# Kernel tuning notes

Hardware: AMD Instinct MI355X
Metric: run time of the kernel (lower is better)

Reference implementation:

```python
import jax, jax.numpy as jnp
import numpy as np
from math import sqrt

HEADS = 16
D_MODEL = 1024
HEAD_DIM = D_MODEL // HEADS  # 64
B, SEQ = 2, 2048


def setup_inputs() -> dict:
    key = jax.random.key(0)
    ks = jax.random.split(key, 8)
    k = jax.random.normal(ks[0], (B, SEQ, D_MODEL), dtype=jnp.float32)
    q = jax.random.normal(ks[1], (B, SEQ, D_MODEL), dtype=jnp.float32)
    v = jax.random.normal(ks[2], (B, SEQ, D_MODEL), dtype=jnp.float32)
    # causal mask, broadcast over batch and heads; masked_fill where mask == 0
    mask = jnp.tril(jnp.ones((SEQ, SEQ), dtype=jnp.int32))[None, None, :, :]
    s = 1.0 / sqrt(HEAD_DIM)
    Wq = jax.random.normal(ks[3], (HEAD_DIM, HEAD_DIM), dtype=jnp.float32) * s
    Wk = jax.random.normal(ks[4], (HEAD_DIM, HEAD_DIM), dtype=jnp.float32) * s
    Wv = jax.random.normal(ks[5], (HEAD_DIM, HEAD_DIM), dtype=jnp.float32) * s
    Wo = jax.random.normal(ks[6], (D_MODEL, D_MODEL), dtype=jnp.float32) * (1.0 / sqrt(D_MODEL))
    bo = jax.random.normal(ks[7], (D_MODEL,), dtype=jnp.float32) * 0.01
    return {"key": k, "query": q, "value": v, "mask": mask,
            "Wq": Wq, "Wk": Wk, "Wv": Wv, "Wo": Wo, "bo": bo}


def reference(key, query, value, mask, Wq, Wk, Wv, Wo, bo):
    b, q_len, d = query.shape
    k_len = key.shape[1]
    hd = d // HEADS
    # reshape to [b, len, heads, head_dim]
    k = key.reshape(b, k_len, HEADS, hd)
    q = query.reshape(b, q_len, HEADS, hd)
    v = value.reshape(b, k_len, HEADS, hd)
    # per-head-dim Linear (weights shared across heads); torch Linear: y = x @ W.T
    k = jnp.einsum('bkhd,ed->bkhe', k, Wk)
    q = jnp.einsum('bqhd,ed->bqhe', q, Wq)
    v = jnp.einsum('bvhd,ed->bvhe', v, Wv)
    # full attention matrix [b, h, q, k]
    product = jnp.einsum('bqhd,bkhd->bhqk', q, k)
    # NOTE: original masks BEFORE scaling by 1/sqrt(head_dim)
    product = jnp.where(mask == 0, jnp.float32(-1e20), product)
    product = product / jnp.float32(sqrt(hd))
    score = jax.nn.softmax(product, axis=-1)
    out = jnp.einsum('bhqv,bvhd->bqhd', score, v).reshape(b, q_len, d)
    out = out @ Wo.T + bo
    return out
```

## Files before the change

kernel.cpp:

```cpp
#include <hip/hip_runtime.h>

typedef __bf16 bf16x8 __attribute__((ext_vector_type(8)));
typedef float  f32x4  __attribute__((ext_vector_type(4)));
typedef unsigned int uint32x4 __attribute__((ext_vector_type(4)));

#define MFMA16(a, b, c) __builtin_amdgcn_mfma_f32_16x16x32_bf16((a), (b), (c), 0, 0, 0)

constexpr int SEQ = 2048;
constexpr int DM  = 1024;
constexpr int NH  = 16;
constexpr int HD  = 64;
constexpr int BATCH = 2;


__device__ inline bf16x8 ld8_f32(const float* p) {
    f32x4 a = *(const f32x4*)p;
    f32x4 b = *(const f32x4*)(p + 4);
    bf16x8 r;
    r[0] = (__bf16)a[0]; r[1] = (__bf16)a[1]; r[2] = (__bf16)a[2]; r[3] = (__bf16)a[3];
    r[4] = (__bf16)b[0]; r[5] = (__bf16)b[1]; r[6] = (__bf16)b[2]; r[7] = (__bf16)b[3];
    return r;
}

__global__ __launch_bounds__(256)
void proj_kernel(const float* __restrict__ Xq, const float* __restrict__ Xk,
                 const float* __restrict__ Xv,
                 const float* __restrict__ Wq, const float* __restrict__ Wk,
                 const float* __restrict__ Wv,
                 __bf16* __restrict__ Qp, __bf16* __restrict__ Kp,
                 __bf16* __restrict__ Vp)
{
    const int tid  = threadIdx.x;
    const int w    = tid >> 6;
    const int lane = tid & 63;
    const int quad = lane >> 4;
    const int l16  = lane & 15;
    const int sblk = blockIdx.x;
    const int bh   = blockIdx.y;
    const int tz   = blockIdx.z;

    const float* X = (tz == 0) ? Xq : (tz == 1) ? Xk : Xv;
    const float* W = (tz == 0) ? Wq : (tz == 1) ? Wk : Wv;
    __bf16*      O = (tz == 0) ? Qp : (tz == 1) ? Kp : Vp;
    const float scale = (tz == 0) ? (0.125f * 1.44269504088896f) : 1.0f;

    const int b = bh >> 4, h = bh & 15;
    const int mrow = sblk * 64 + w * 16 + l16;

    const size_t xoff = (size_t)(b * SEQ + mrow) * DM + h * HD + quad * 8;
    bf16x8 a0 = ld8_f32(X + xoff);
    bf16x8 a1 = ld8_f32(X + xoff + 32);

    f32x4 acc[4];
    #pragma unroll
    for (int nt = 0; nt < 4; ++nt) {
        const size_t woff = (size_t)(nt * 16 + l16) * HD + quad * 8;
        bf16x8 b0 = ld8_f32(W + woff);
        bf16x8 b1 = ld8_f32(W + woff + 32);
        f32x4 c = {0.f, 0.f, 0.f, 0.f};
        c = MFMA16(a0, b0, c);
        c = MFMA16(a1, b1, c);
        acc[nt] = c;
    }

    __bf16* obase = O + (size_t)bh * SEQ * HD;
    #pragma unroll
    for (int nt = 0; nt < 4; ++nt) {
        #pragma unroll
        for (int r = 0; r < 4; ++r) {
            const int srow = sblk * 64 + w * 16 + quad * 4 + r;
            obase[(size_t)srow * HD + nt * 16 + l16] = (__bf16)(acc[nt][r] * scale);
        }
    }
}

__global__ __launch_bounds__(256, 2)
void attn_kernel(const __bf16* __restrict__ Qp, const __bf16* __restrict__ Kp,
                 const __bf16* __restrict__ Vp, __bf16* __restrict__ AO)
{
    __shared__ __align__(16) unsigned int K_lds[2][64 * 36];
    __shared__ __align__(16) unsigned int VT2[2][64 * 36];
    __shared__ __align__(16) __bf16 P_lds[4][16 * 72];

    const int tid  = threadIdx.x;
    const int w    = tid >> 6;
    const int lane = tid & 63;
    const int quad = lane >> 4;
    const int l16  = lane & 15;
    const int pr   = blockIdx.x;
    const int bh   = blockIdx.y;

    const __bf16* Qb = Qp + (size_t)bh * SEQ * HD;
    const __bf16* Kb = Kp + (size_t)bh * SEQ * HD;
    const __bf16* Vb = Vp + (size_t)bh * SEQ * HD;

    bf16x8 onesf;
    #pragma unroll
    for (int i = 0; i < 8; ++i) onesf[i] = (l16 == 0) ? (__bf16)1.0f : (__bf16)0.0f;

    const int krow = tid >> 3, kcol = tid & 7;
    const int jp = tid & 31, d0 = (tid >> 5) * 8;

    #pragma unroll
    for (int phase = 0; phase < 2; ++phase) {
        const int tile = (phase == 0) ? (31 - pr) : pr;
        const int q0   = tile * 64;
        const int nkc  = tile + 1;

        __syncthreads();

        const int mrow = q0 + w * 16 + l16;
        bf16x8 qa0 = *(const bf16x8*)(Qb + (size_t)mrow * HD + quad * 8);
        bf16x8 qa1 = *(const bf16x8*)(Qb + (size_t)mrow * HD + quad * 8 + 32);

        f32x4 accO[4];
        #pragma unroll
        for (int nt = 0; nt < 4; ++nt) { f32x4 z = {0.f,0.f,0.f,0.f}; accO[nt] = z; }
        f32x4 acc5 = {0.f, 0.f, 0.f, 0.f};

        uint32x4 kpre0 = *(const uint32x4*)(Kb + (size_t)krow * HD + kcol * 8);
        uint32x4 kpre1 = *(const uint32x4*)(Kb + (size_t)(krow + 32) * HD + kcol * 8);
        uint32x4 vlo   = *(const uint32x4*)(Vb + (size_t)(2 * jp) * HD + d0);
        uint32x4 vhi   = *(const uint32x4*)(Vb + (size_t)(2 * jp + 1) * HD + d0);

        for (int kc = 0; kc < nkc; ++kc) {
            const int buf = kc & 1;
            *(uint32x4*)&K_lds[buf][krow * 36 + kcol * 4]        = kpre0;
            *(uint32x4*)&K_lds[buf][(krow + 32) * 36 + kcol * 4] = kpre1;
            #pragma unroll
            for (int i2 = 0; i2 < 4; ++i2) {
                const unsigned int va = vlo[i2], vb = vhi[i2];
                VT2[buf][(d0 + 2 * i2    ) * 36 + jp] = (va & 0xffffu) | (vb << 16);
                VT2[buf][(d0 + 2 * i2 + 1) * 36 + jp] = (va >> 16) | (vb & 0xffff0000u);
            }
            __syncthreads();

            if (kc + 1 < nkc) {
                const size_t o = (size_t)(kc + 1) * 64;
                kpre0 = *(const uint32x4*)(Kb + (o + krow) * HD + kcol * 8);
                kpre1 = *(const uint32x4*)(Kb + (o + krow + 32) * HD + kcol * 8);
                vlo   = *(const uint32x4*)(Vb + (o + 2 * jp) * HD + d0);
                vhi   = *(const uint32x4*)(Vb + (o + 2 * jp + 1) * HD + d0);
            }

            f32x4 s[4];
            #pragma unroll
            for (int nt = 0; nt < 4; ++nt) {
                const unsigned int* kb = &K_lds[buf][(nt * 16 + l16) * 36 + quad * 4];
                bf16x8 kb0 = *(const bf16x8*)(kb);
                bf16x8 kb1 = *(const bf16x8*)(kb + 16);
                f32x4 c = {0.f, 0.f, 0.f, 0.f};
                c = MFMA16(qa0, kb0, c);
                c = MFMA16(qa1, kb1, c);
                s[nt] = c;
            }
            if (kc == tile) {
                #pragma unroll
                for (int nt = 0; nt < 4; ++nt) {
                    const int j = kc * 64 + nt * 16 + l16;
                    #pragma unroll
                    for (int r = 0; r < 4; ++r) {
                        const int qrow = q0 + w * 16 + quad * 4 + r;
                        if (j > qrow) s[nt][r] = -1e30f;
                    }
                }
            }
            #pragma unroll
            for (int nt = 0; nt < 4; ++nt) {
                #pragma unroll
                for (int r = 0; r < 4; ++r) {
                    P_lds[w][(quad * 4 + r) * 72 + nt * 16 + l16] =
                        (__bf16)exp2f(s[nt][r]);
                }
            }
            asm volatile("" ::: "memory");
            bf16x8 pa0 = *(const bf16x8*)&P_lds[w][l16 * 72 + quad * 8];
            bf16x8 pa1 = *(const bf16x8*)&P_lds[w][l16 * 72 + quad * 8 + 32];
            #pragma unroll
            for (int nt = 0; nt < 4; ++nt) {
                const unsigned int* vb2 = &VT2[buf][(nt * 16 + l16) * 36 + quad * 4];
                bf16x8 vb0 = *(const bf16x8*)(vb2);
                bf16x8 vb1 = *(const bf16x8*)(vb2 + 16);
                accO[nt] = MFMA16(pa0, vb0, accO[nt]);
                accO[nt] = MFMA16(pa1, vb1, accO[nt]);
            }
            acc5 = MFMA16(pa0, onesf, acc5);
            acc5 = MFMA16(pa1, onesf, acc5);
        }

        const int b = bh >> 4, h = bh & 15;
        float inv[4];
        #pragma unroll
        for (int r = 0; r < 4; ++r) {
            const float ls = __shfl(acc5[r], quad * 16, 64);
            inv[r] = 1.0f / ls;
        }
        #pragma unroll
        for (int nt = 0; nt < 4; ++nt) {
            #pragma unroll
            for (int r = 0; r < 4; ++r) {
                const int qrow = q0 + w * 16 + quad * 4 + r;
                AO[(size_t)(b * SEQ + qrow) * DM + h * HD + nt * 16 + l16] =
                    (__bf16)(accO[nt][r] * inv[r]);
            }
        }
    }
}

__global__ __launch_bounds__(256)
void wconv_kernel(const float* __restrict__ Wo, __bf16* __restrict__ Wb)
{
    const size_t i = ((size_t)blockIdx.x * 256 + threadIdx.x) * 8;
    *(bf16x8*)(Wb + i) = ld8_f32(Wo + i);
}

__global__ __launch_bounds__(256)
void ogemm_kernel(const __bf16* __restrict__ AO, const __bf16* __restrict__ Wb,
                  const float* __restrict__ bo, float* __restrict__ out)
{
    __shared__ __align__(16) unsigned int A_lds[2][64 * 36];
    __shared__ __align__(16) unsigned int B_lds[2][128 * 36];

    const int tid  = threadIdx.x;
    const int w    = tid >> 6;
    const int lane = tid & 63;
    const int quad = lane >> 4;
    const int l16  = lane & 15;
    const int m0   = blockIdx.x * 64;
    const int n0   = blockIdx.y * 128;

    const int row = tid >> 3, c = tid & 7;

    f32x4 acc[8];
    #pragma unroll
    for (int nt = 0; nt < 8; ++nt) { f32x4 z = {0.f,0.f,0.f,0.f}; acc[nt] = z; }

    uint32x4 apre[2], bpre[4];
    #pragma unroll
    for (int i = 0; i < 2; ++i)
        apre[i] = *(const uint32x4*)(AO + (size_t)(m0 + row + i * 32) * DM + c * 8);
    #pragma unroll
    for (int i = 0; i < 4; ++i)
        bpre[i] = *(const uint32x4*)(Wb + (size_t)(n0 + row + i * 32) * DM + c * 8);

    for (int kc = 0; kc < DM / 64; ++kc) {
        const int buf = kc & 1;
        #pragma unroll
        for (int i = 0; i < 2; ++i)
            *(uint32x4*)&A_lds[buf][(row + i * 32) * 36 + c * 4] = apre[i];
        #pragma unroll
        for (int i = 0; i < 4; ++i)
            *(uint32x4*)&B_lds[buf][(row + i * 32) * 36 + c * 4] = bpre[i];
        __syncthreads();

        if (kc + 1 < DM / 64) {
            const size_t o = (size_t)(kc + 1) * 64;
            #pragma unroll
            for (int i = 0; i < 2; ++i)
                apre[i] = *(const uint32x4*)(AO + (size_t)(m0 + row + i * 32) * DM + o + c * 8);
            #pragma unroll
            for (int i = 0; i < 4; ++i)
                bpre[i] = *(const uint32x4*)(Wb + (size_t)(n0 + row + i * 32) * DM + o + c * 8);
        }

        #pragma unroll
        for (int ks = 0; ks < 2; ++ks) {
            bf16x8 a = *(const bf16x8*)&A_lds[buf][(w * 16 + l16) * 36 + ks * 16 + quad * 4];
            #pragma unroll
            for (int nt = 0; nt < 8; ++nt) {
                bf16x8 bb = *(const bf16x8*)&B_lds[buf][(nt * 16 + l16) * 36 + ks * 16 + quad * 4];
                acc[nt] = MFMA16(a, bb, acc[nt]);
            }
        }
    }

    #pragma unroll
    for (int nt = 0; nt < 8; ++nt) {
        const int n = n0 + nt * 16 + l16;
        const float bof = bo[n];
        #pragma unroll
        for (int r = 0; r < 4; ++r) {
            const int m = m0 + w * 16 + quad * 4 + r;
            out[(size_t)m * DM + n] = acc[nt][r] + bof;
        }
    }
}

extern "C" void kernel_launch(void* const* d_in, const int* in_sizes, int n_in,
                              void* d_out, int out_size, void* d_ws, size_t ws_size,
                              hipStream_t stream)
{
    const float* key   = (const float*)d_in[0];
    const float* query = (const float*)d_in[1];
    const float* value = (const float*)d_in[2];
    const float* Wq = (const float*)d_in[4];
    const float* Wk = (const float*)d_in[5];
    const float* Wv = (const float*)d_in[6];
    const float* Wo = (const float*)d_in[7];
    const float* bo = (const float*)d_in[8];

    const size_t per = (size_t)BATCH * NH * SEQ * HD;
    __bf16* Qp = (__bf16*)d_ws;
    __bf16* Kp = Qp + per;
    __bf16* Vp = Kp + per;
    __bf16* AO = Vp + per;
    __bf16* Wb = Kp;

    proj_kernel<<<dim3(SEQ / 64, BATCH * NH, 3), 256, 0, stream>>>(
        query, key, value, Wq, Wk, Wv, Qp, Kp, Vp);
    attn_kernel<<<dim3(SEQ / 128, BATCH * NH), 256, 0, stream>>>(Qp, Kp, Vp, AO);
    wconv_kernel<<<dim3(DM * DM / (256 * 8)), 256, 0, stream>>>(Wo, Wb);
    ogemm_kernel<<<dim3(BATCH * SEQ / 64, DM / 128), 256, 0, stream>>>(
        AO, Wb, bo, (float*)d_out);
}
```

Baseline: 196.5 us.

## Switch attention to 32x32 MFMA with register-resident P and split-K warps

After: 194.6 us. Within noise of the previous version (-1.0%).

```diff
diff --git a/kernel.cpp b/kernel.cpp
--- a/kernel.cpp
+++ b/kernel.cpp
@@ -2,16 +2,20 @@
 
 typedef __bf16 bf16x8 __attribute__((ext_vector_type(8)));
 typedef float  f32x4  __attribute__((ext_vector_type(4)));
+typedef float  f32x16 __attribute__((ext_vector_type(16)));
 typedef unsigned int uint32x4 __attribute__((ext_vector_type(4)));
 
 #define MFMA16(a, b, c) __builtin_amdgcn_mfma_f32_16x16x32_bf16((a), (b), (c), 0, 0, 0)
+#define MFMA32(a, b, c) __builtin_amdgcn_mfma_f32_32x32x16_bf16((a), (b), (c), 0, 0, 0)
+
+#define CVTPK(d, x, y) asm("v_cvt_pk_bf16_f32 %0, %1, %2" : "=v"(d) : "v"(x), "v"(y))
+#define PLSWAP(a, b)   asm("v_permlane32_swap_b32 %0, %1" : "+v"(a), "+v"(b))
 
 constexpr int SEQ = 2048;
 constexpr int DM  = 1024;
 constexpr int NH  = 16;
 constexpr int HD  = 64;
 constexpr int BATCH = 2;
-
 
 __device__ inline bf16x8 ld8_f32(const float* p) {
     f32x4 a = *(const f32x4*)p;
@@ -80,23 +84,20 @@
 {
     __shared__ __align__(16) unsigned int K_lds[2][64 * 36];
     __shared__ __align__(16) unsigned int VT2[2][64 * 36];
-    __shared__ __align__(16) __bf16 P_lds[4][16 * 72];
 
     const int tid  = threadIdx.x;
     const int w    = tid >> 6;
     const int lane = tid & 63;
-    const int quad = lane >> 4;
-    const int l16  = lane & 15;
+    const int hi   = lane >> 5;
+    const int l32  = lane & 31;
+    const int qg   = w >> 1;
+    const int kg   = w & 1;
     const int pr   = blockIdx.x;
     const int bh   = blockIdx.y;
 
     const __bf16* Qb = Qp + (size_t)bh * SEQ * HD;
     const __bf16* Kb = Kp + (size_t)bh * SEQ * HD;
     const __bf16* Vb = Vp + (size_t)bh * SEQ * HD;
-
-    bf16x8 onesf;
-    #pragma unroll
-    for (int i = 0; i < 8; ++i) onesf[i] = (l16 == 0) ? (__bf16)1.0f : (__bf16)0.0f;
 
     const int krow = tid >> 3, kcol = tid & 7;
     const int jp = tid & 31, d0 = (tid >> 5) * 8;
@@ -109,14 +110,19 @@
 
         __syncthreads();
 
-        const int mrow = q0 + w * 16 + l16;
-        bf16x8 qa0 = *(const bf16x8*)(Qb + (size_t)mrow * HD + quad * 8);
-        bf16x8 qa1 = *(const bf16x8*)(Qb + (size_t)mrow * HD + quad * 8 + 32);
-
-        f32x4 accO[4];
-        #pragma unroll
-        for (int nt = 0; nt < 4; ++nt) { f32x4 z = {0.f,0.f,0.f,0.f}; accO[nt] = z; }
-        f32x4 acc5 = {0.f, 0.f, 0.f, 0.f};
+        const __bf16* qp = Qb + (size_t)(q0 + 32 * qg + l32) * HD + hi * 8;
+        const bf16x8 qb0 = *(const bf16x8*)(qp);
+        const bf16x8 qb1 = *(const bf16x8*)(qp + 16);
+        const bf16x8 qb2 = *(const bf16x8*)(qp + 32);
+        const bf16x8 qb3 = *(const bf16x8*)(qp + 48);
+
+        f32x16 accO[2];
+        #pragma unroll
+        for (int et = 0; et < 2; ++et) {
+            #pragma unroll
+            for (int r = 0; r < 16; ++r) accO[et][r] = 0.f;
+        }
+        float rs0 = 0.f, rs1 = 0.f;
 
         uint32x4 kpre0 = *(const uint32x4*)(Kb + (size_t)krow * HD + kcol * 8);
         uint32x4 kpre1 = *(const uint32x4*)(Kb + (size_t)(krow + 32) * HD + kcol * 8);
@@ -143,65 +149,76 @@
                 vhi   = *(const uint32x4*)(Vb + (o + 2 * jp + 1) * HD + d0);
             }
 
-            f32x4 s[4];
-            #pragma unroll
-            for (int nt = 0; nt < 4; ++nt) {
-                const unsigned int* kb = &K_lds[buf][(nt * 16 + l16) * 36 + quad * 4];
-                bf16x8 kb0 = *(const bf16x8*)(kb);
-                bf16x8 kb1 = *(const bf16x8*)(kb + 16);
-                f32x4 c = {0.f, 0.f, 0.f, 0.f};
-                c = MFMA16(qa0, kb0, c);
-                c = MFMA16(qa1, kb1, c);
-                s[nt] = c;
-            }
-            if (kc == tile) {
+            if (!(kc == tile && qg == 0 && kg == 1)) {
+                const __bf16* kp = (const __bf16*)&K_lds[buf][(32 * kg + l32) * 36] + hi * 8;
+                f32x16 s;
                 #pragma unroll
-                for (int nt = 0; nt < 4; ++nt) {
-                    const int j = kc * 64 + nt * 16 + l16;
+                for (int r = 0; r < 16; ++r) s[r] = 0.f;
+                s = MFMA32(*(const bf16x8*)(kp),      qb0, s);
+                s = MFMA32(*(const bf16x8*)(kp + 16), qb1, s);
+                s = MFMA32(*(const bf16x8*)(kp + 32), qb2, s);
+                s = MFMA32(*(const bf16x8*)(kp + 48), qb3, s);
+
+                if (kc == tile && qg == kg) {
                     #pragma unroll
-                    for (int r = 0; r < 4; ++r) {
-                        const int qrow = q0 + w * 16 + quad * 4 + r;
-                        if (j > qrow) s[nt][r] = -1e30f;
+                    for (int r = 0; r < 16; ++r) {
+                        const int cr = (r & 3) + 8 * (r >> 2) + 4 * hi;
+                        if (cr > l32) s[r] = -1e30f;
                     }
                 }
-            }
-            #pragma unroll
-            for (int nt = 0; nt < 4; ++nt) {
+
+                float p[16];
                 #pragma unroll
-                for (int r = 0; r < 4; ++r) {
-                    P_lds[w][(quad * 4 + r) * 72 + nt * 16 + l16] =
-                        (__bf16)exp2f(s[nt][r]);
+                for (int r = 0; r < 16; ++r) p[r] = exp2f(s[r]);
+                #pragma unroll
+                for (int r = 0; r < 8; ++r) { rs0 += p[2 * r]; rs1 += p[2 * r + 1]; }
+
+                unsigned int w0, w1, w2, w3, w4, w5, w6, w7;
+                CVTPK(w0, p[0],  p[1]);  CVTPK(w1, p[2],  p[3]);
+                CVTPK(w2, p[4],  p[5]);  CVTPK(w3, p[6],  p[7]);
+                CVTPK(w4, p[8],  p[9]);  CVTPK(w5, p[10], p[11]);
+                CVTPK(w6, p[12], p[13]); CVTPK(w7, p[14], p[15]);
+                PLSWAP(w0, w2); PLSWAP(w1, w3); PLSWAP(w4, w6); PLSWAP(w5, w7);
+                uint32x4 u0 = {w0, w1, w2, w3};
+                uint32x4 u1 = {w4, w5, w6, w7};
+                const bf16x8 pa0 = *(const bf16x8*)&u0;
+                const bf16x8 pa1 = *(const bf16x8*)&u1;
+
+                #pragma unroll
+                for (int et = 0; et < 2; ++et) {
+                    const __bf16* vp = (const __bf16*)&VT2[buf][(et * 32 + l32) * 36]
+                                       + 32 * kg + hi * 8;
+                    accO[et] = MFMA32(pa0, *(const bf16x8*)(vp),      accO[et]);
+                    accO[et] = MFMA32(pa1, *(const bf16x8*)(vp + 16), accO[et]);
                 }
             }
-            asm volatile("" ::: "memory");
-            bf16x8 pa0 = *(const bf16x8*)&P_lds[w][l16 * 72 + quad * 8];
-            bf16x8 pa1 = *(const bf16x8*)&P_lds[w][l16 * 72 + quad * 8 + 32];
-            #pragma unroll
-            for (int nt = 0; nt < 4; ++nt) {
-                const unsigned int* vb2 = &VT2[buf][(nt * 16 + l16) * 36 + quad * 4];
-                bf16x8 vb0 = *(const bf16x8*)(vb2);
-                bf16x8 vb1 = *(const bf16x8*)(vb2 + 16);
-                accO[nt] = MFMA16(pa0, vb0, accO[nt]);
-                accO[nt] = MFMA16(pa1, vb1, accO[nt]);
-            }
-            acc5 = MFMA16(pa0, onesf, acc5);
-            acc5 = MFMA16(pa1, onesf, acc5);
-        }
-
-        const int b = bh >> 4, h = bh & 15;
-        float inv[4];
-        #pragma unroll
-        for (int r = 0; r < 4; ++r) {
-            const float ls = __shfl(acc5[r], quad * 16, 64);
-            inv[r] = 1.0f / ls;
-        }
-        #pragma unroll
-        for (int nt = 0; nt < 4; ++nt) {
-            #pragma unroll
-            for (int r = 0; r < 4; ++r) {
-                const int qrow = q0 + w * 16 + quad * 4 + r;
-                AO[(size_t)(b * SEQ + qrow) * DM + h * HD + nt * 16 + l16] =
-                    (__bf16)(accO[nt][r] * inv[r]);
+        }
+
+        __syncthreads();
+        float* red = (float*)K_lds;
+        float rsum = rs0 + rs1;
+        if (kg == 1) {
+            float* dst = red + (size_t)(qg * 64 + lane) * 33;
+            #pragma unroll
+            for (int r = 0; r < 16; ++r) { dst[r] = accO[0][r]; dst[16 + r] = accO[1][r]; }
+            dst[32] = rsum;
+        }
+        __syncthreads();
+        if (kg == 0) {
+            const float* src = red + (size_t)(qg * 64 + lane) * 33;
+            #pragma unroll
+            for (int r = 0; r < 16; ++r) { accO[0][r] += src[r]; accO[1][r] += src[16 + r]; }
+            rsum += src[32];
+            const float rt  = rsum + __shfl_xor(rsum, 32, 64);
+            const float ivq = 1.0f / rt;
+            const int b = bh >> 4, h = bh & 15;
+            #pragma unroll
+            for (int r = 0; r < 16; ++r) {
+                const int cr = (r & 3) + 8 * (r >> 2) + 4 * hi;
+                const float iv = __shfl(ivq, cr, 64);
+                __bf16* ao = AO + (size_t)(b * SEQ + q0 + 32 * qg + cr) * DM + h * HD;
+                ao[l32]      = (__bf16)(accO[0][r] * iv);
+                ao[32 + l32] = (__bf16)(accO[1][r] * iv);
             }
         }
     }
```
